# Kernel optimization log

Hardware: AMD Instinct MI355X
Metric: run time of the kernel (lower is better)

The kernel has to match this reference:

```python
import jax, jax.numpy as jnp
import numpy as np

IN_F, OUT_F = 4096, 4096
WBITS, GS, OFI = 3, 128, 128          # bitwidth, group_size, outfeature_interval
NG, NB = IN_F // GS, OUT_F // OFI     # 32 groups x 32 out-blocks
WPB = WBITS * GS * OFI // 32          # int32 words per (group, out-block) = 1536


def setup_inputs() -> dict:
    key = jax.random.key(0)
    k = jax.random.split(key, 6)
    x = jax.random.normal(k[0], (1, 128, IN_F), jnp.float32)
    qweight = jax.random.randint(k[1], (NG * NB * WPB,), 0, 2**31 - 1, jnp.int32)
    alpha = 0.02 * jax.random.uniform(k[2], (NG, OUT_F), jnp.float32) + 0.001
    beta = 0.001 * jax.random.normal(k[3], (NG, OUT_F), jnp.float32)
    block_bitwidth = jnp.full((NG, NB), WBITS, dtype=jnp.int32)   # uniform bitwidth
    offset = jnp.arange(NG * NB, dtype=jnp.int32) * WPB           # word start per block
    in_reorder = jax.random.permutation(k[4], IN_F).astype(jnp.int32)
    out_reorder = jax.random.permutation(k[5], OUT_F).astype(jnp.int32)
    return dict(x=x, qweight=qweight, alpha=alpha, beta=beta,
                block_bitwidth=block_bitwidth, offset=offset,
                in_reorder=in_reorder, out_reorder=out_reorder)


def _dequant(qweight, alpha, beta, offset):
    # gather each block's packed words via its offset
    idx = offset[:, None] + jnp.arange(WPB, dtype=jnp.int32)      # (NG*NB, WPB)
    words = qweight[idx].reshape(NG, NB, WBITS, GS * OFI // 32)
    # unpack 32 bits per word -> +-1 binary codes per bit-plane
    bits = (words[..., None] >> jnp.arange(32, dtype=jnp.int32)) & 1
    codes = bits.reshape(NG, NB, WBITS, GS, OFI).astype(jnp.float32) * 2.0 - 1.0
    plane = (2.0 ** jnp.arange(WBITS)).astype(jnp.float32)        # bit-plane weights
    q = jnp.einsum('gnbio,b->gnio', codes, plane)                 # (NG,NB,GS,OFI)
    a = alpha.reshape(NG, NB, OFI)[:, :, None, :]
    bt = beta.reshape(NG, NB, OFI)[:, :, None, :]
    w = q * a + bt                                                # per-group scale/shift
    return w.transpose(0, 2, 1, 3).reshape(IN_F, OUT_F)


def reference(x, qweight, alpha, beta, block_bitwidth, offset, in_reorder, out_reorder):
    # block_bitwidth is uniform (== WBITS) in this reference; dequant closes over WBITS
    w = _dequant(qweight, alpha, beta, offset)                    # (IN_F, OUT_F)
    B, T, _ = x.shape
    xf = x.reshape(-1, IN_F)[:, in_reorder]                       # input permutation
    y = (xf @ w)[:, out_reorder]                                  # matmul + out permutation
    return y.reshape(B, T, OUT_F)
```

## Files before the change

### kernel.cpp

```cpp
#include <hip/hip_runtime.h>
#include <hip/hip_bf16.h>
#include <stdint.h>

#define IN_F   4096
#define OUT_F  4096
#define NGRP   32
#define NBLK   32
#define GSZ    128
#define OFI    128
#define WPB    1536
#define M_TOK  128
#define KSPLIT 8
#define NTILE  64

typedef __attribute__((ext_vector_type(8))) short bf16x8;
typedef __attribute__((ext_vector_type(4))) float f32x4;

static __device__ __forceinline__ unsigned cvt_pk_bf16(float lo, float hi) {
    unsigned r;
    asm("v_cvt_pk_bf16_f32 %0, %1, %2" : "=v"(r) : "v"(lo), "v"(hi));
    return r;
}

static __device__ __forceinline__ float u_as_f(unsigned u) {
    union { unsigned u; float f; } v; v.u = u; return v.f;
}

static __device__ __forceinline__ void gload_lds16(const void* g, void* s) {
    __builtin_amdgcn_global_load_lds(
        (const __attribute__((address_space(1))) unsigned int*)g,
        (__attribute__((address_space(3))) unsigned int*)s, 16, 0, 0);
}

__global__ __launch_bounds__(256) void k_prep(const float* __restrict__ x,
                                              const int* __restrict__ in_reorder,
                                              const int* __restrict__ out_reorder,
                                              const float* __restrict__ alpha,
                                              const float* __restrict__ beta,
                                              unsigned short* __restrict__ xr,
                                              int* __restrict__ inv_out,
                                              float* __restrict__ A2,
                                              float* __restrict__ Bp) {
    int b = blockIdx.x;
    if (b < 256) {
        int idx = b * 256 + threadIdx.x;
        int t  = idx >> 9;
        int i0 = (idx & 511) << 3;
        int4 s0 = *(const int4*)&in_reorder[i0];
        int4 s1 = *(const int4*)&in_reorder[i0 + 4];
        const float* row = x + (size_t)t * IN_F;
        float v0 = row[s0.x], v1 = row[s0.y], v2 = row[s0.z], v3 = row[s0.w];
        float v4 = row[s1.x], v5 = row[s1.y], v6 = row[s1.z], v7 = row[s1.w];
        uint4 pk;
        pk.x = cvt_pk_bf16(v0, v1);
        pk.y = cvt_pk_bf16(v2, v3);
        pk.z = cvt_pk_bf16(v4, v5);
        pk.w = cvt_pk_bf16(v6, v7);
        *(uint4*)&xr[(size_t)t * IN_F + i0] = pk;
    } else if (b < 260) {
        int i0 = ((b - 256) * 256 + threadIdx.x) << 2;
        int4 o = *(const int4*)&out_reorder[i0];
        inv_out[o.x] = i0;
        inv_out[o.y] = i0 + 1;
        inv_out[o.z] = i0 + 2;
        inv_out[o.w] = i0 + 3;
    } else {
        int idx = ((b - 260) * 256 + threadIdx.x) << 2;
        float4 a = *(const float4*)&alpha[idx];
        float4 bt = *(const float4*)&beta[idx];
        float4 a2 = make_float4(2.f * a.x, 2.f * a.y, 2.f * a.z, 2.f * a.w);
        float4 bp = make_float4(bt.x - 135.f * a.x, bt.y - 135.f * a.y,
                                bt.z - 135.f * a.z, bt.w - 135.f * a.w);
        *(float4*)&A2[idx] = a2;
        *(float4*)&Bp[idx] = bp;
    }
}

__global__ __launch_bounds__(256, 2) void k_fused(const unsigned short* __restrict__ xr,
                                                  const int* __restrict__ qweight,
                                                  const float* __restrict__ A2,
                                                  const float* __restrict__ Bp,
                                                  const int* __restrict__ offset,
                                                  float* __restrict__ Cpart) {
    __shared__ unsigned short Alds[128 * 128];
    __shared__ unsigned short Blds[NTILE * 128];
    const int nb  = blockIdx.x;
    const int ks  = blockIdx.y;
    const int n   = nb >> 1;
    const int wcb = (nb & 1) * 2;
    const int n0  = nb * NTILE;
    const int tid = threadIdx.x;
    const int l   = tid & 63;
    const int wid = tid >> 6;
    const int wm  = wid >> 1;
    const int wn  = wid & 1;

    const int p  = tid >> 2;
    const int wc = (tid >> 1) & 1;
    const int h  = tid & 1;
    const int wq = wcb + wc;
    const int io0 = 2 * p;

    const int rl = l >> 4;
    const int cl = l & 15;

    f32x4 acc[4][2] = {};

    int cw0a, cw0b, cw1a, cw1b, cw2a, cw2b;
    {
        const int gb0 = (ks * 4) * NBLK + n;
        const int* q = qweight + offset[gb0];
        cw0a = q[ io0      * 4 + wq];
        cw0b = q[(io0 + 1) * 4 + wq];
        cw1a = q[ io0      * 4 + wq + 512];
        cw1b = q[(io0 + 1) * 4 + wq + 512];
        cw2a = q[ io0      * 4 + wq + 1024];
        cw2b = q[(io0 + 1) * 4 + wq + 1024];
    }

    #pragma unroll
    for (int kt = 0; kt < 4; ++kt) {
        const int g  = ks * 4 + kt;
        const int k0 = g * GSZ;

        #pragma unroll
        for (int i = 0; i < 8; ++i) {
            int R = wid * 32 + i * 4 + rl;
            const unsigned short* src = xr + ((size_t)R << 12) + k0 + ((cl ^ (R & 15)) << 3);
            gload_lds16(src, (char*)Alds + wid * 8192 + i * 1024);
        }

        {
            const float* a2 = A2 + g * OUT_F + n0 + wc * 32 + h * 16;
            const float* bp = Bp + g * OUT_F + n0 + wc * 32 + h * 16;
            unsigned* B32 = (unsigned*)Blds;
            #pragma unroll
            for (int j = 0; j < 16; ++j) {
                int jb  = h * 16 + j;
                int col = wc * 32 + jb;
                float sa = a2[j];
                float sb = bp[j];
                unsigned na  = ((cw0a >> jb) & 1) | (((cw1a >> jb) & 1) << 1) | (((cw2a >> jb) & 1) << 2);
                unsigned nbq = ((cw0b >> jb) & 1) | (((cw1b >> jb) & 1) << 1) | (((cw2b >> jb) & 1) << 2);
                float va = fmaf(u_as_f(0x42800000u | (na  << 17)), sa, sb);
                float vb = fmaf(u_as_f(0x42800000u | (nbq << 17)), sa, sb);
                B32[col * 64 + (((p >> 2) ^ (col & 15)) << 2) + (p & 3)] = cvt_pk_bf16(va, vb);
            }
        }
        __syncthreads();

        if (kt < 3) {
            const int gb1 = (ks * 4 + kt + 1) * NBLK + n;
            const int* q = qweight + offset[gb1];
            cw0a = q[ io0      * 4 + wq];
            cw0b = q[(io0 + 1) * 4 + wq];
            cw1a = q[ io0      * 4 + wq + 512];
            cw1b = q[(io0 + 1) * 4 + wq + 512];
            cw2a = q[ io0      * 4 + wq + 1024];
            cw2b = q[(io0 + 1) * 4 + wq + 1024];
        }

        #pragma unroll
        for (int kk = 0; kk < 4; ++kk) {
            const int cb = kk * 4 + (l >> 4);
            bf16x8 af[4], bfr[2];
            #pragma unroll
            for (int m = 0; m < 4; ++m) {
                int row = wm * 64 + m * 16 + (l & 15);
                af[m] = *(const bf16x8*)&Alds[row * 128 + ((cb ^ (row & 15)) << 3)];
            }
            #pragma unroll
            for (int nn = 0; nn < 2; ++nn) {
                int clr = wn * 32 + nn * 16 + (l & 15);
                bfr[nn] = *(const bf16x8*)&Blds[clr * 128 + ((cb ^ (clr & 15)) << 3)];
            }
            #pragma unroll
            for (int m = 0; m < 4; ++m)
                #pragma unroll
                for (int nn = 0; nn < 2; ++nn)
                    acc[m][nn] = __builtin_amdgcn_mfma_f32_16x16x32_bf16(
                        af[m], bfr[nn], acc[m][nn], 0, 0, 0);
        }
        __syncthreads();
    }

    float* Cb = Cpart + (size_t)ks * (M_TOK * OUT_F);
    #pragma unroll
    for (int m = 0; m < 4; ++m) {
        int row = wm * 64 + m * 16 + ((l >> 4) << 2);
        #pragma unroll
        for (int nn = 0; nn < 2; ++nn) {
            int col = n0 + wn * 32 + nn * 16 + (l & 15);
            #pragma unroll
            for (int r = 0; r < 4; ++r)
                Cb[(size_t)(row + r) * OUT_F + col] = acc[m][nn][r];
        }
    }
}

__global__ __launch_bounds__(256) void k_reduce(const float* __restrict__ Cpart,
                                                const int* __restrict__ inv_out,
                                                float* __restrict__ out) {
    int idx = blockIdx.x * 256 + threadIdx.x;
    int t  = idx >> 10;
    int c0 = (idx & 1023) << 2;
    float4 s = make_float4(0.f, 0.f, 0.f, 0.f);
    #pragma unroll
    for (int ks = 0; ks < KSPLIT; ++ks) {
        float4 v = *(const float4*)&Cpart[(size_t)ks * (M_TOK * OUT_F) + (size_t)t * OUT_F + c0];
        s.x += v.x; s.y += v.y; s.z += v.z; s.w += v.w;
    }
    const int* op = &inv_out[c0];
    float* row = out + (size_t)t * OUT_F;
    row[op[0]] = s.x;
    row[op[1]] = s.y;
    row[op[2]] = s.z;
    row[op[3]] = s.w;
}

extern "C" void kernel_launch(void* const* d_in, const int* in_sizes, int n_in,
                              void* d_out, int out_size, void* d_ws, size_t ws_size,
                              hipStream_t stream) {
    const float* x           = (const float*)d_in[0];
    const int*   qweight     = (const int*)d_in[1];
    const float* alpha       = (const float*)d_in[2];
    const float* beta        = (const float*)d_in[3];
    const int*   offset      = (const int*)d_in[5];
    const int*   in_reorder  = (const int*)d_in[6];
    const int*   out_reorder = (const int*)d_in[7];
    float* out = (float*)d_out;

    char* ws = (char*)d_ws;
    unsigned short* xr      = (unsigned short*)ws;
    float*          Cpart   = (float*)(ws + (1u << 20));
    int*            inv_out = (int*)(ws + (1u << 20) + (16u << 20));
    float*          A2      = (float*)(ws + (1u << 20) + (16u << 20) + (16u << 10));
    float*          Bp      = A2 + NGRP * OUT_F;

    k_prep<<<dim3(388), dim3(256), 0, stream>>>(x, in_reorder, out_reorder,
                                                alpha, beta, xr, inv_out, A2, Bp);
    k_fused<<<dim3(64, KSPLIT), dim3(256), 0, stream>>>(xr, qweight, A2, Bp, offset, Cpart);
    k_reduce<<<dim3(512), dim3(256), 0, stream>>>(Cpart, inv_out, out);
}
```

Before: 33.52 us.

## Double-buffer dequantized weights, widen N tile to 128, read activations from global

Each block now covers a full 128-wide output block instead of 64, so the grid halves to 256 blocks. Dequantized weight tiles are double-buffered in LDS, letting the next group's dequant overlap the current group's MFMAs, and each iteration needs one barrier instead of two. The activation tile is no longer staged in LDS; MFMA operands are loaded directly from global memory through the cache, which is uncoalesced and redundant across waves. Fewer blocks (one per CU via launch bounds) also lowers parallelism on a 256-CU part.

```diff
diff --git a/kernel.cpp b/kernel.cpp
--- a/kernel.cpp
+++ b/kernel.cpp
@@ -11,7 +11,6 @@
 #define WPB    1536
 #define M_TOK  128
 #define KSPLIT 8
-#define NTILE  64
 
 typedef __attribute__((ext_vector_type(8))) short bf16x8;
 typedef __attribute__((ext_vector_type(4))) float f32x4;
@@ -24,12 +23,6 @@
 
 static __device__ __forceinline__ float u_as_f(unsigned u) {
     union { unsigned u; float f; } v; v.u = u; return v.f;
-}
-
-static __device__ __forceinline__ void gload_lds16(const void* g, void* s) {
-    __builtin_amdgcn_global_load_lds(
-        (const __attribute__((address_space(1))) unsigned int*)g,
-        (__attribute__((address_space(3))) unsigned int*)s, 16, 0, 0);
 }
 
 __global__ __launch_bounds__(256) void k_prep(const float* __restrict__ x,
@@ -76,121 +69,122 @@
     }
 }
 
-__global__ __launch_bounds__(256, 2) void k_fused(const unsigned short* __restrict__ xr,
+__global__ __launch_bounds__(256, 1) void k_fused(const unsigned short* __restrict__ xr,
                                                   const int* __restrict__ qweight,
                                                   const float* __restrict__ A2,
                                                   const float* __restrict__ Bp,
                                                   const int* __restrict__ offset,
                                                   float* __restrict__ Cpart) {
-    __shared__ unsigned short Alds[128 * 128];
-    __shared__ unsigned short Blds[NTILE * 128];
+    __shared__ unsigned short Blds[2][OFI * 128];
     const int nb  = blockIdx.x;
     const int ks  = blockIdx.y;
-    const int n   = nb >> 1;
-    const int wcb = (nb & 1) * 2;
-    const int n0  = nb * NTILE;
+    const int n0  = nb * OFI;
     const int tid = threadIdx.x;
     const int l   = tid & 63;
     const int wid = tid >> 6;
     const int wm  = wid >> 1;
     const int wn  = wid & 1;
 
-    const int p  = tid >> 2;
-    const int wc = (tid >> 1) & 1;
-    const int h  = tid & 1;
-    const int wq = wcb + wc;
+    const int p   = tid >> 2;
+    const int wc  = tid & 3;
     const int io0 = 2 * p;
 
-    const int rl = l >> 4;
-    const int cl = l & 15;
-
-    f32x4 acc[4][2] = {};
-
-    int cw0a, cw0b, cw1a, cw1b, cw2a, cw2b;
+    f32x4 acc[4][4] = {};
+
+    const int g0 = ks * 4;
+    int w[2][6];
+
     {
-        const int gb0 = (ks * 4) * NBLK + n;
-        const int* q = qweight + offset[gb0];
-        cw0a = q[ io0      * 4 + wq];
-        cw0b = q[(io0 + 1) * 4 + wq];
-        cw1a = q[ io0      * 4 + wq + 512];
-        cw1b = q[(io0 + 1) * 4 + wq + 512];
-        cw2a = q[ io0      * 4 + wq + 1024];
-        cw2b = q[(io0 + 1) * 4 + wq + 1024];
-    }
+        const int* q = qweight + offset[g0 * NBLK + nb];
+        w[0][0] = q[ io0      * 4 + wc];
+        w[0][1] = q[(io0 + 1) * 4 + wc];
+        w[0][2] = q[ io0      * 4 + wc + 512];
+        w[0][3] = q[(io0 + 1) * 4 + wc + 512];
+        w[0][4] = q[ io0      * 4 + wc + 1024];
+        w[0][5] = q[(io0 + 1) * 4 + wc + 1024];
+    }
+
+    #define DEQUANT(gg, ww, buf)                                                     \
+    {                                                                                \
+        const float* a2 = A2 + (gg) * OUT_F + n0 + wc * 32;                          \
+        const float* bp = Bp + (gg) * OUT_F + n0 + wc * 32;                          \
+        unsigned* B32 = (unsigned*)Blds[buf];                                        \
+        _Pragma("unroll")                                                            \
+        for (int j = 0; j < 32; ++j) {                                               \
+            int col = wc * 32 + j;                                                   \
+            float sa = a2[j];                                                        \
+            float sb = bp[j];                                                        \
+            unsigned na  = ((ww[0] >> j) & 1) | (((ww[2] >> j) & 1) << 1)            \
+                         | (((ww[4] >> j) & 1) << 2);                                \
+            unsigned nbq = ((ww[1] >> j) & 1) | (((ww[3] >> j) & 1) << 1)            \
+                         | (((ww[5] >> j) & 1) << 2);                                \
+            float va = fmaf(u_as_f(0x42800000u | (na  << 17)), sa, sb);              \
+            float vb = fmaf(u_as_f(0x42800000u | (nbq << 17)), sa, sb);              \
+            B32[col * 64 + (((p >> 2) ^ (col & 15)) << 2) + (p & 3)]                 \
+                = cvt_pk_bf16(va, vb);                                               \
+        }                                                                            \
+    }
+
+    DEQUANT(g0, w[0], 0);
+    {
+        const int* q = qweight + offset[(g0 + 1) * NBLK + nb];
+        w[1][0] = q[ io0      * 4 + wc];
+        w[1][1] = q[(io0 + 1) * 4 + wc];
+        w[1][2] = q[ io0      * 4 + wc + 512];
+        w[1][3] = q[(io0 + 1) * 4 + wc + 512];
+        w[1][4] = q[ io0      * 4 + wc + 1024];
+        w[1][5] = q[(io0 + 1) * 4 + wc + 1024];
+    }
+    __syncthreads();
 
     #pragma unroll
     for (int kt = 0; kt < 4; ++kt) {
-        const int g  = ks * 4 + kt;
-        const int k0 = g * GSZ;
-
-        #pragma unroll
-        for (int i = 0; i < 8; ++i) {
-            int R = wid * 32 + i * 4 + rl;
-            const unsigned short* src = xr + ((size_t)R << 12) + k0 + ((cl ^ (R & 15)) << 3);
-            gload_lds16(src, (char*)Alds + wid * 8192 + i * 1024);
+        if (kt < 3)
+            DEQUANT(g0 + kt + 1, w[(kt + 1) & 1], (kt + 1) & 1);
+        if (kt < 2) {
+            const int* q = qweight + offset[(g0 + kt + 2) * NBLK + nb];
+            w[kt & 1][0] = q[ io0      * 4 + wc];
+            w[kt & 1][1] = q[(io0 + 1) * 4 + wc];
+            w[kt & 1][2] = q[ io0      * 4 + wc + 512];
+            w[kt & 1][3] = q[(io0 + 1) * 4 + wc + 512];
+            w[kt & 1][4] = q[ io0      * 4 + wc + 1024];
+            w[kt & 1][5] = q[(io0 + 1) * 4 + wc + 1024];
         }
 
-        {
-            const float* a2 = A2 + g * OUT_F + n0 + wc * 32 + h * 16;
-            const float* bp = Bp + g * OUT_F + n0 + wc * 32 + h * 16;
-            unsigned* B32 = (unsigned*)Blds;
-            #pragma unroll
-            for (int j = 0; j < 16; ++j) {
-                int jb  = h * 16 + j;
-                int col = wc * 32 + jb;
-                float sa = a2[j];
-                float sb = bp[j];
-                unsigned na  = ((cw0a >> jb) & 1) | (((cw1a >> jb) & 1) << 1) | (((cw2a >> jb) & 1) << 2);
-                unsigned nbq = ((cw0b >> jb) & 1) | (((cw1b >> jb) & 1) << 1) | (((cw2b >> jb) & 1) << 2);
-                float va = fmaf(u_as_f(0x42800000u | (na  << 17)), sa, sb);
-                float vb = fmaf(u_as_f(0x42800000u | (nbq << 17)), sa, sb);
-                B32[col * 64 + (((p >> 2) ^ (col & 15)) << 2) + (p & 3)] = cvt_pk_bf16(va, vb);
-            }
-        }
-        __syncthreads();
-
-        if (kt < 3) {
-            const int gb1 = (ks * 4 + kt + 1) * NBLK + n;
-            const int* q = qweight + offset[gb1];
-            cw0a = q[ io0      * 4 + wq];
-            cw0b = q[(io0 + 1) * 4 + wq];
-            cw1a = q[ io0      * 4 + wq + 512];
-            cw1b = q[(io0 + 1) * 4 + wq + 512];
-            cw2a = q[ io0      * 4 + wq + 1024];
-            cw2b = q[(io0 + 1) * 4 + wq + 1024];
-        }
-
+        const int k0 = (g0 + kt) * GSZ;
+        const unsigned short* Bl = Blds[kt & 1];
         #pragma unroll
         for (int kk = 0; kk < 4; ++kk) {
             const int cb = kk * 4 + (l >> 4);
-            bf16x8 af[4], bfr[2];
+            bf16x8 af[4], bfr[4];
             #pragma unroll
             for (int m = 0; m < 4; ++m) {
                 int row = wm * 64 + m * 16 + (l & 15);
-                af[m] = *(const bf16x8*)&Alds[row * 128 + ((cb ^ (row & 15)) << 3)];
+                af[m] = *(const bf16x8*)&xr[(size_t)row * IN_F + k0 + (cb << 3)];
             }
             #pragma unroll
-            for (int nn = 0; nn < 2; ++nn) {
-                int clr = wn * 32 + nn * 16 + (l & 15);
-                bfr[nn] = *(const bf16x8*)&Blds[clr * 128 + ((cb ^ (clr & 15)) << 3)];
+            for (int nn = 0; nn < 4; ++nn) {
+                int colr = wn * 64 + nn * 16 + (l & 15);
+                bfr[nn] = *(const bf16x8*)&Bl[colr * 128 + ((cb ^ (colr & 15)) << 3)];
             }
             #pragma unroll
             for (int m = 0; m < 4; ++m)
                 #pragma unroll
-                for (int nn = 0; nn < 2; ++nn)
+                for (int nn = 0; nn < 4; ++nn)
                     acc[m][nn] = __builtin_amdgcn_mfma_f32_16x16x32_bf16(
                         af[m], bfr[nn], acc[m][nn], 0, 0, 0);
         }
-        __syncthreads();
-    }
+        if (kt < 3) __syncthreads();
+    }
+    #undef DEQUANT
 
     float* Cb = Cpart + (size_t)ks * (M_TOK * OUT_F);
     #pragma unroll
     for (int m = 0; m < 4; ++m) {
         int row = wm * 64 + m * 16 + ((l >> 4) << 2);
         #pragma unroll
-        for (int nn = 0; nn < 2; ++nn) {
-            int col = n0 + wn * 32 + nn * 16 + (l & 15);
+        for (int nn = 0; nn < 4; ++nn) {
+            int col = n0 + wn * 64 + nn * 16 + (l & 15);
             #pragma unroll
             for (int r = 0; r < 4; ++r)
                 Cb[(size_t)(row + r) * OUT_F + col] = acc[m][nn][r];
@@ -239,6 +233,6 @@
 
     k_prep<<<dim3(388), dim3(256), 0, stream>>>(x, in_reorder, out_reorder,
                                                 alpha, beta, xr, inv_out, A2, Bp);
-    k_fused<<<dim3(64, KSPLIT), dim3(256), 0, stream>>>(xr, qweight, A2, Bp, offset, Cpart);
+    k_fused<<<dim3(32, KSPLIT), dim3(256), 0, stream>>>(xr, qweight, A2, Bp, offset, Cpart);
     k_reduce<<<dim3(512), dim3(256), 0, stream>>>(Cpart, inv_out, out);
 }
```

Result: slower. 40.35 us (+20.4%).

## Fuse split-K reduction into GEMM via last-block atomic counter

Applied to the files above, without the earlier changes.

Drops the separate reduce kernel. Each output-column tile now bumps an atomic counter after writing its partial sums, and the last of the 8 K-split blocks sums all partials and scatters the permuted output. The counters are zeroed by an extra block in the prep kernel. The A-tile load switches from direct global-to-LDS loads to plain vector loads plus LDS stores, and the barrier is moved after the next weight prefetch. This saves one launch but makes the final reduction run on only 64 blocks, and the register-staged A load may cost more than the async path.

```diff
diff --git a/kernel.cpp b/kernel.cpp
--- a/kernel.cpp
+++ b/kernel.cpp
@@ -26,12 +26,6 @@
     union { unsigned u; float f; } v; v.u = u; return v.f;
 }
 
-static __device__ __forceinline__ void gload_lds16(const void* g, void* s) {
-    __builtin_amdgcn_global_load_lds(
-        (const __attribute__((address_space(1))) unsigned int*)g,
-        (__attribute__((address_space(3))) unsigned int*)s, 16, 0, 0);
-}
-
 __global__ __launch_bounds__(256) void k_prep(const float* __restrict__ x,
                                               const int* __restrict__ in_reorder,
                                               const int* __restrict__ out_reorder,
@@ -40,7 +34,8 @@
                                               unsigned short* __restrict__ xr,
                                               int* __restrict__ inv_out,
                                               float* __restrict__ A2,
-                                              float* __restrict__ Bp) {
+                                              float* __restrict__ Bp,
+                                              int* __restrict__ done) {
     int b = blockIdx.x;
     if (b < 256) {
         int idx = b * 256 + threadIdx.x;
@@ -64,7 +59,7 @@
         inv_out[o.y] = i0 + 1;
         inv_out[o.z] = i0 + 2;
         inv_out[o.w] = i0 + 3;
-    } else {
+    } else if (b < 388) {
         int idx = ((b - 260) * 256 + threadIdx.x) << 2;
         float4 a = *(const float4*)&alpha[idx];
         float4 bt = *(const float4*)&beta[idx];
@@ -73,6 +68,8 @@
                                 bt.z - 135.f * a.z, bt.w - 135.f * a.w);
         *(float4*)&A2[idx] = a2;
         *(float4*)&Bp[idx] = bp;
+    } else {
+        if (threadIdx.x < 64) done[threadIdx.x] = 0;
     }
 }
 
@@ -81,9 +78,13 @@
                                                   const float* __restrict__ A2,
                                                   const float* __restrict__ Bp,
                                                   const int* __restrict__ offset,
-                                                  float* __restrict__ Cpart) {
+                                                  float* __restrict__ Cpart,
+                                                  const int* __restrict__ inv_out,
+                                                  int* __restrict__ done,
+                                                  float* __restrict__ out) {
     __shared__ unsigned short Alds[128 * 128];
     __shared__ unsigned short Blds[NTILE * 128];
+    __shared__ int is_last;
     const int nb  = blockIdx.x;
     const int ks  = blockIdx.y;
     const int n   = nb >> 1;
@@ -101,9 +102,6 @@
     const int wq = wcb + wc;
     const int io0 = 2 * p;
 
-    const int rl = l >> 4;
-    const int cl = l & 15;
-
     f32x4 acc[4][2] = {};
 
     int cw0a, cw0b, cw1a, cw1b, cw2a, cw2b;
@@ -124,10 +122,12 @@
         const int k0 = g * GSZ;
 
         #pragma unroll
-        for (int i = 0; i < 8; ++i) {
-            int R = wid * 32 + i * 4 + rl;
-            const unsigned short* src = xr + ((size_t)R << 12) + k0 + ((cl ^ (R & 15)) << 3);
-            gload_lds16(src, (char*)Alds + wid * 8192 + i * 1024);
+        for (int c = 0; c < 8; ++c) {
+            int e   = (c * 256 + tid) * 8;
+            int row = e >> 7;
+            int cb  = (e >> 3) & 15;
+            uint4 v = *(const uint4*)&xr[(size_t)row * IN_F + k0 + (cb << 3)];
+            *(uint4*)&Alds[row * 128 + ((cb ^ (row & 15)) << 3)] = v;
         }
 
         {
@@ -147,7 +147,6 @@
                 B32[col * 64 + (((p >> 2) ^ (col & 15)) << 2) + (p & 3)] = cvt_pk_bf16(va, vb);
             }
         }
-        __syncthreads();
 
         if (kt < 3) {
             const int gb1 = (ks * 4 + kt + 1) * NBLK + n;
@@ -159,6 +158,7 @@
             cw2a = q[ io0      * 4 + wq + 1024];
             cw2b = q[(io0 + 1) * 4 + wq + 1024];
         }
+        __syncthreads();
 
         #pragma unroll
         for (int kk = 0; kk < 4; ++kk) {
@@ -196,26 +196,37 @@
                 Cb[(size_t)(row + r) * OUT_F + col] = acc[m][nn][r];
         }
     }
-}
-
-__global__ __launch_bounds__(256) void k_reduce(const float* __restrict__ Cpart,
-                                                const int* __restrict__ inv_out,
-                                                float* __restrict__ out) {
-    int idx = blockIdx.x * 256 + threadIdx.x;
-    int t  = idx >> 10;
-    int c0 = (idx & 1023) << 2;
-    float4 s = make_float4(0.f, 0.f, 0.f, 0.f);
-    #pragma unroll
-    for (int ks = 0; ks < KSPLIT; ++ks) {
-        float4 v = *(const float4*)&Cpart[(size_t)ks * (M_TOK * OUT_F) + (size_t)t * OUT_F + c0];
-        s.x += v.x; s.y += v.y; s.z += v.z; s.w += v.w;
-    }
-    const int* op = &inv_out[c0];
-    float* row = out + (size_t)t * OUT_F;
-    row[op[0]] = s.x;
-    row[op[1]] = s.y;
-    row[op[2]] = s.z;
-    row[op[3]] = s.w;
+
+    __threadfence();
+    __syncthreads();
+    if (tid == 0) {
+        int prev = __hip_atomic_fetch_add(&done[nb], 1, __ATOMIC_ACQ_REL,
+                                          __HIP_MEMORY_SCOPE_AGENT);
+        is_last = (prev == KSPLIT - 1);
+    }
+    __syncthreads();
+    if (is_last) {
+        __threadfence();
+        #pragma unroll
+        for (int qq = 0; qq < 8; ++qq) {
+            int task = qq * 256 + tid;
+            int t  = task >> 4;
+            int c  = n0 + ((task & 15) << 2);
+            float4 s = make_float4(0.f, 0.f, 0.f, 0.f);
+            #pragma unroll
+            for (int k2 = 0; k2 < KSPLIT; ++k2) {
+                float4 v = *(const float4*)&Cpart[(size_t)k2 * (M_TOK * OUT_F)
+                                                  + (size_t)t * OUT_F + c];
+                s.x += v.x; s.y += v.y; s.z += v.z; s.w += v.w;
+            }
+            const int* op = &inv_out[c];
+            float* row = out + (size_t)t * OUT_F;
+            row[op[0]] = s.x;
+            row[op[1]] = s.y;
+            row[op[2]] = s.z;
+            row[op[3]] = s.w;
+        }
+    }
 }
 
 extern "C" void kernel_launch(void* const* d_in, const int* in_sizes, int n_in,
@@ -232,13 +243,14 @@
 
     char* ws = (char*)d_ws;
     unsigned short* xr      = (unsigned short*)ws;
-    float*          Cpart   = (float*)(ws + (1u << 20));
-    int*            inv_out = (int*)(ws + (1u << 20) + (16u << 20));
-    float*          A2      = (float*)(ws + (1u << 20) + (16u << 20) + (16u << 10));
-    float*          Bp      = A2 + NGRP * OUT_F;
-
-    k_prep<<<dim3(388), dim3(256), 0, stream>>>(x, in_reorder, out_reorder,
-                                                alpha, beta, xr, inv_out, A2, Bp);
-    k_fused<<<dim3(64, KSPLIT), dim3(256), 0, stream>>>(xr, qweight, A2, Bp, offset, Cpart);
-    k_reduce<<<dim3(512), dim3(256), 0, stream>>>(Cpart, inv_out, out);
-}
+    float*          Cpart   = (float*)(ws + 0x100000);
+    int*            inv_out = (int*)(ws + 0x1100000);
+    float*          A2      = (float*)(ws + 0x1104000);
+    float*          Bp      = (float*)(ws + 0x1184000);
+    int*            done    = (int*)(ws + 0x1204000);
+
+    k_prep<<<dim3(389), dim3(256), 0, stream>>>(x, in_reorder, out_reorder,
+                                                alpha, beta, xr, inv_out, A2, Bp, done);
+    k_fused<<<dim3(64, KSPLIT), dim3(256), 0, stream>>>(xr, qweight, A2, Bp, offset,
+                                                        Cpart, inv_out, done, out);
+}
```

New measurement: 110.0 us. 228% more time.
